# Performance work log

Measured on AMD Instinct MI355X. Metric: run time of the kernel, lower is better.

Reference implementation:

```python
import jax, jax.numpy as jnp
import numpy as np

HEADS = 8
DIM_HEAD = 64
LA = 0.33
LD = 0.33
LG = 0.33


def setup_inputs() -> dict:
    key = jax.random.key(0)
    ks = jax.random.split(key, 6)
    B, N, D = 4, 1024, 512
    inner = HEADS * DIM_HEAD
    x = jax.random.normal(ks[0], (B, N, D), jnp.float32)
    mask = jax.random.uniform(ks[1], (B, N)) < 0.9
    # sparse 0/1 molecular adjacency
    adjacency_mat = (jax.random.uniform(ks[2], (B, N, N)) < 0.05).astype(jnp.float32)
    # positive pairwise distances
    distance_mat = jax.random.uniform(ks[3], (B, N, N), jnp.float32) * 5.0
    W_qkv = jax.random.normal(ks[4], (D, inner * 3), jnp.float32) * 0.02
    W_out = jax.random.normal(ks[5], (inner, D), jnp.float32) * 0.02
    b_out = jnp.zeros((D,), jnp.float32)
    return {"x": x, "mask": mask, "adjacency_mat": adjacency_mat,
            "distance_mat": distance_mat, "W_qkv": W_qkv, "W_out": W_out, "b_out": b_out}


def reference(x, mask, adjacency_mat, distance_mat, W_qkv, W_out, b_out):
    B, N, _ = x.shape
    scale = DIM_HEAD ** -0.5
    # 'b n (h qkv d)' split: reshape to (B, N, H, 3, Dh) then move heads forward
    qkv = (x @ W_qkv).reshape(B, N, HEADS, 3, DIM_HEAD)
    q, k, v = (jnp.transpose(qkv[..., i, :], (0, 2, 1, 3)) for i in range(3))
    dots = jnp.einsum('bhid,bhjd->bhij', q, k) * scale  # [B,H,N,N]
    big = jnp.finfo(dots.dtype).max
    m2 = mask[:, None, :, None] & mask[:, None, None, :]  # [B,1,N,N]
    dots = jnp.where(m2, dots, -big)
    attn = jax.nn.softmax(dots, axis=-1) * LA
    # adjacency masked to 0; distance masked to +max so exp(-t) -> 0
    adj = jnp.where(m2, adjacency_mat[:, None], 0.0)
    dist = jnp.where(m2, distance_mat[:, None], big)
    attn = attn + LG * adj + LD * jnp.exp(-dist)
    out = jnp.einsum('bhij,bhjd->bhid', attn, v)
    out = jnp.transpose(out, (0, 2, 1, 3)).reshape(B, N, HEADS * DIM_HEAD)
    return out @ W_out + b_out
```

## Files before the change

### kernel.cpp

```cpp
#include <hip/hip_runtime.h>
#include <hip/hip_bf16.h>

typedef __attribute__((ext_vector_type(8))) __bf16 bf16x8;
typedef __attribute__((ext_vector_type(8))) unsigned short ushort8;
typedef __attribute__((ext_vector_type(4))) float f32x4;

#define DEVFN static __device__ __forceinline__

constexpr int B_ = 4, N_ = 1024, H_ = 8, DH_ = 64, INNER_ = 512, QC_ = 1536;
constexpr int JS_ = 2;
constexpr float LA_ = 0.33f, LD_ = 0.33f, LG_ = 0.33f;
constexpr float SCALE2_ = 0.125f * 1.44269504088896f;
constexpr long OCP_STRIDE_ = (long)4096 * 512;
constexpr long LP_STRIDE_  = (long)4 * 8 * 1024;

DEVFN unsigned short f2b(float f){
  unsigned int u = __builtin_bit_cast(unsigned int, f);
  u += 0x7FFFu + ((u >> 16) & 1u);
  return (unsigned short)(u >> 16);
}
DEVFN float b2f(unsigned short s){
  unsigned int u = ((unsigned int)s) << 16;
  return __builtin_bit_cast(float, u);
}
DEVFN float fexp2(float x){
  float r; asm("v_exp_f32 %0, %1" : "=v"(r) : "v"(x)); return r;
}
DEVFN unsigned int pack2(float lo, float hi){
  union { unsigned int u; __bf16 h[2]; } z;
  z.h[0] = (__bf16)lo; z.h[1] = (__bf16)hi;
  return z.u;
}

DEVFN f32x4 mfma16(bf16x8 a, bf16x8 b, f32x4 c){
  return __builtin_amdgcn_mfma_f32_16x16x32_bf16(a, b, c, 0, 0, 0);
}

DEVFN bf16x8 ldsb8(const unsigned short* p){ return *(const bf16x8*)p; }

DEVFN void gload16(const unsigned short* g, unsigned short* l){
  __builtin_amdgcn_global_load_lds(
      (const __attribute__((address_space(1))) unsigned int*)g,
      (__attribute__((address_space(3))) unsigned int*)l, 16, 0, 0);
}

DEVFN void lds_barrier(){
  __builtin_amdgcn_sched_barrier(0);
  asm volatile("s_waitcnt lgkmcnt(0)\n\ts_barrier" ::: "memory");
  __builtin_amdgcn_sched_barrier(0);
}


DEVFN int detect_enc_w0(const unsigned char* m8, const int* m32, const float* mf,
                        int t, int* fsh){
  if (t < 64){
    unsigned char a = m8[t];
    int bb = m32[t];
    float c = mf[t];
    unsigned long long bad0 = __ballot(a > 1);
    unsigned long long one0 = __ballot(a == 1);
    unsigned long long bad1 = __ballot(bb != 0 && bb != 1);
    unsigned long long one1 = __ballot(bb == 1);
    unsigned long long bad2 = __ballot(c != 0.0f && c != 1.0f);
    unsigned long long one2 = __ballot(c == 1.0f);
    if (t == 0){
      int f = 0;
      if (bad0 == 0ull && __popcll(one0) > 42) f = 0;
      else if (bad1 == 0ull && __popcll(one1) > 42) f = 1;
      else if (bad2 == 0ull && __popcll(one2) > 42) f = 2;
      *fsh = f;
    }
  }
  __syncthreads();
  return *fsh;
}

__global__ void prep_k(const unsigned char* __restrict__ m8, const int* __restrict__ m32,
                       const float* __restrict__ mf, unsigned char* __restrict__ mv,
                       const float* __restrict__ x, unsigned short* __restrict__ xb,
                       const float* __restrict__ Wq, unsigned short* __restrict__ WqT,
                       const float* __restrict__ Wo, unsigned short* __restrict__ WoT)
{
  const int bid = blockIdx.x, t = threadIdx.x;
  if (bid < 16){
    __shared__ int fsh;
    int f = detect_enc_w0(m8, m32, mf, t, &fsh);
    int i = bid * 256 + t;
    unsigned char v;
    if (f == 0) v = (m8[i] != 0);
    else if (f == 1) v = (m32[i] != 0);
    else v = (mf[i] != 0.0f);
    mv[i] = v;
  } else if (bid < 2064){
    int i = (bid - 16) * 256 + t;
    float4 v = ((const float4*)x)[i];
    ushort4 o = { f2b(v.x), f2b(v.y), f2b(v.z), f2b(v.w) };
    ((ushort4*)xb)[i] = o;
  } else {
    const float* W; unsigned short* Wt; int K, Nn, bx, by;
    if (bid < 2832){ W = Wq; Wt = WqT; K = 512; Nn = 1536; int r = bid - 2064; bx = r % 48; by = r / 48; }
    else           { W = Wo; Wt = WoT; K = 512; Nn = 512;  int r = bid - 2832; bx = r % 16; by = r / 16; }
    __shared__ float tt[32][33];
    int nb = bx * 32, kb = by * 32;
    int tx = t & 31, ty = t >> 5;
    #pragma unroll
    for (int i = 0; i < 32; i += 8)
      tt[ty + i][tx] = W[(long)(kb + ty + i) * Nn + nb + tx];
    __syncthreads();
    #pragma unroll
    for (int i = 0; i < 32; i += 8)
      Wt[(long)(nb + ty + i) * K + kb + tx] = f2b(tt[tx][ty + i]);
  }
}

template<int MODE, int BM, int BN>
__global__ __launch_bounds__(256)
void gemm_bt_k(const unsigned short* __restrict__ A, const unsigned short* __restrict__ Bt,
               const float* __restrict__ Cin, void* __restrict__ Cout,
               const unsigned short* __restrict__ Op, const float* __restrict__ Lp,
               unsigned short* __restrict__ VtOut,
               int M, int Nn, int K, long azs, long bzs)
{
  constexpr int BK = 64;
  constexpr int WM = BM / 2, WN = BN / 2, MR = WM / 16, NR = WN / 16;
  __shared__ __attribute__((aligned(16))) unsigned short As[2][BM * BK];
  __shared__ __attribute__((aligned(16))) unsigned short Bs[2][BN * BK];
  const int bm = blockIdx.x * BM, bn = blockIdx.y * BN, z = blockIdx.z;
  const unsigned short* Ap = A + (long)z * azs;
  const unsigned short* Bp = Bt + (long)z * bzs;
  const int tid = threadIdx.x, w = tid >> 6, lane = tid & 63;
  const int l15 = lane & 15, lg = lane >> 4;
  const int wr = w >> 1, wc = w & 1;
  const int srow = lane >> 3;
  const int sk0 = ((lane & 7) ^ srow) * 8;
  const int rk0 = (lg ^ (l15 & 7)) * 8;
  const int rk1 = ((lg + 4) ^ (l15 & 7)) * 8;

  f32x4 acc[MR][NR] = {};

  for (int kk = 0;;){
    if (kk == 0){
      #pragma unroll
      for (int i = 0; i < BM / 32; i++){
        int r0 = i * 32 + w * 8;
        gload16(Ap + (long)(bm + r0 + srow) * K + sk0, &As[0][r0 * BK]);
      }
      #pragma unroll
      for (int i = 0; i < BN / 32; i++){
        int r0 = i * 32 + w * 8;
        gload16(Bp + (long)(bn + r0 + srow) * K + sk0, &Bs[0][r0 * BK]);
      }
      __syncthreads();
    }
    int cur = (kk / BK) & 1;
    if (kk + BK < K){
      #pragma unroll
      for (int i = 0; i < BM / 32; i++){
        int r0 = i * 32 + w * 8;
        gload16(Ap + (long)(bm + r0 + srow) * K + (kk + BK) + sk0, &As[cur ^ 1][r0 * BK]);
      }
      #pragma unroll
      for (int i = 0; i < BN / 32; i++){
        int r0 = i * 32 + w * 8;
        gload16(Bp + (long)(bn + r0 + srow) * K + (kk + BK) + sk0, &Bs[cur ^ 1][r0 * BK]);
      }
    }
    bf16x8 af[MR][2], bf[NR][2];
    #pragma unroll
    for (int m = 0; m < MR; m++){
      const unsigned short* p = &As[cur][(wr * WM + m * 16 + l15) * BK];
      af[m][0] = ldsb8(p + rk0); af[m][1] = ldsb8(p + rk1);
    }
    #pragma unroll
    for (int n = 0; n < NR; n++){
      const unsigned short* p = &Bs[cur][(wc * WN + n * 16 + l15) * BK];
      bf[n][0] = ldsb8(p + rk0); bf[n][1] = ldsb8(p + rk1);
    }
    #pragma unroll
    for (int m = 0; m < MR; m++)
      #pragma unroll
      for (int n = 0; n < NR; n++){
        acc[m][n] = mfma16(af[m][0], bf[n][0], acc[m][n]);
        acc[m][n] = mfma16(af[m][1], bf[n][1], acc[m][n]);
      }
    kk += BK;
    if (kk >= K) break;
    __syncthreads();
  }

  #pragma unroll
  for (int m = 0; m < MR; m++)
    #pragma unroll
    for (int n = 0; n < NR; n++){
      int row0 = bm + wr * WM + m * 16 + lg * 4;
      int col = bn + wc * WN + n * 16 + l15;
      if (MODE == 0){
        ushort4 o;
        unsigned short* op = (unsigned short*)&o;
        #pragma unroll
        for (int r = 0; r < 4; r++){
          op[r] = f2b(acc[m][n][r]);
          ((unsigned short*)Cout)[(long)(row0 + r) * Nn + col] = op[r];
        }
        int hm = col % 192;
        if (hm >= 128){
          int bb = row0 >> 10, j0 = row0 & (N_ - 1);
          int hd = (col / 192) * 64 + (hm - 128);
          *(ushort4*)(VtOut + ((long)bb * INNER_ + hd) * N_ + j0) = o;
        }
      } else if (MODE == 1){
        #pragma unroll
        for (int r = 0; r < 4; r++){
          int row = row0 + r;
          float v = acc[m][n][r];
          long obase = ((long)z * N_ + row) * INNER_ + col;
          long lbase = ((long)z * H_ + (col >> 6)) * N_ + row;
          float o = 0.f, l = 0.f;
          #pragma unroll
          for (int js = 0; js < JS_; js++){
            o += b2f(Op[js * OCP_STRIDE_ + obase]);
            l += Lp[js * LP_STRIDE_ + lbase];
          }
          v += LA_ * o / l;
          ((unsigned short*)Cout)[((long)z * N_ + row) * Nn + col] = f2b(v);
        }
      } else {
        #pragma unroll
        for (int r = 0; r < 4; r++)
          ((float*)Cout)[(long)(row0 + r) * Nn + col] = acc[m][n][r] + Cin[col];
      }
    }
}

__global__ __launch_bounds__(256, 3)
void attn_madd_k(const unsigned short* __restrict__ QKV, const unsigned short* __restrict__ Vt,
                 const unsigned char* __restrict__ mv,
                 unsigned short* __restrict__ Ocp, float* __restrict__ Lp,
                 const unsigned char* __restrict__ m8, const int* __restrict__ m32,
                 const float* __restrict__ mf,
                 const float* __restrict__ adj, const float* __restrict__ dist,
                 unsigned short* __restrict__ Madd)
{
  __shared__ __attribute__((aligned(16))) unsigned short Ks[64][72];
  __shared__ __attribute__((aligned(16))) unsigned short Vs[64][72];
  __shared__ __attribute__((aligned(16))) unsigned short Ps[4][16][72];
  const int bid = blockIdx.x, tid = threadIdx.x;

  if (bid >= 512){
    int f = detect_enc_w0(m8, m32, mf, tid, (int*)&Ps[0][0][0]);
    long i = (long)(bid - 512) * 256 + tid;
    long e = i * 4;
    int b = (int)(e >> 20);
    int rem = (int)(e & (long)(N_ * N_ - 1));
    int row = rem >> 10, col0 = rem & (N_ - 1);
    float4 a = ((const float4*)adj)[i];
    float4 d = ((const float4*)dist)[i];
    bool mi, mc[4];
    if (f == 0){
      mi = m8[b * N_ + row] != 0;
      unsigned int pk = *(const unsigned int*)(m8 + b * N_ + col0);
      #pragma unroll
      for (int r = 0; r < 4; r++) mc[r] = ((pk >> (8 * r)) & 255u) != 0;
    } else if (f == 1){
      mi = m32[b * N_ + row] != 0;
      #pragma unroll
      for (int r = 0; r < 4; r++) mc[r] = m32[b * N_ + col0 + r] != 0;
    } else {
      mi = mf[b * N_ + row] != 0.0f;
      #pragma unroll
      for (int r = 0; r < 4; r++) mc[r] = mf[b * N_ + col0 + r] != 0.0f;
    }
    float va[4] = {a.x, a.y, a.z, a.w};
    float vd[4] = {d.x, d.y, d.z, d.w};
    ushort4 o;
    unsigned short* op = (unsigned short*)&o;
    #pragma unroll
    for (int r = 0; r < 4; r++){
      bool m2 = mi && mc[r];
      float v = m2 ? (LG_ * va[r] + LD_ * __expf(-vd[r])) : 0.0f;
      op[r] = f2b(v);
    }
    ((ushort4*)Madd)[i] = o;
    return;
  }

  const int qb = (bid & 7) * 128, h = (bid >> 3) & 7;
  const int zc = bid >> 6;
  const int b = zc & 3, js = zc >> 2;
  const int w = tid >> 6, lane = tid & 63;
  const int l15 = lane & 15, lg = lane >> 4;

  bf16x8 qf[2][2];
  bool rv[2];
  #pragma unroll
  for (int qg = 0; qg < 2; qg++){
    const long qr = (long)(b * N_ + qb + w * 32 + qg * 16 + l15) * QC_ + h * 192;
    qf[qg][0] = *(const bf16x8*)(QKV + qr + lg * 8);
    qf[qg][1] = *(const bf16x8*)(QKV + qr + 32 + lg * 8);
    rv[qg] = mv[b * N_ + qb + w * 32 + qg * 16 + l15] != 0;
  }

  float l_run[2] = {0.f, 0.f};
  f32x4 acc[2][4] = {};

  const unsigned short* Vbase = Vt + ((long)b * INNER_ + h * DH_) * N_;
  const unsigned short* Kbase = QKV + (long)b * N_ * QC_ + h * 192 + 64;
  const int kr0 = tid >> 3, kr1 = kr0 + 32;
  const int ko = (tid & 7) * 8;
  const int jb0 = js * (N_ / JS_);
  constexpr int NT = N_ / JS_ / 64;

  ushort8 kreg0, kreg1, vreg0, vreg1;
  {
    kreg0 = *(const ushort8*)(Kbase + (long)(jb0 + kr0) * QC_ + ko);
    kreg1 = *(const ushort8*)(Kbase + (long)(jb0 + kr1) * QC_ + ko);
    vreg0 = *(const ushort8*)(Vbase + (long)kr0 * N_ + jb0 + ko);
    vreg1 = *(const ushort8*)(Vbase + (long)kr1 * N_ + jb0 + ko);
  }

  for (int jt = 0; jt < NT; jt++){
    const int jbase = jb0 + jt * 64;
    lds_barrier();
    *(ushort8*)&Ks[kr0][ko] = kreg0;
    *(ushort8*)&Ks[kr1][ko] = kreg1;
    *(ushort8*)&Vs[kr0][ko] = vreg0;
    *(ushort8*)&Vs[kr1][ko] = vreg1;
    if (jt < NT - 1){
      const int jn = jbase + 64;
      kreg0 = *(const ushort8*)(Kbase + (long)(jn + kr0) * QC_ + ko);
      kreg1 = *(const ushort8*)(Kbase + (long)(jn + kr1) * QC_ + ko);
      vreg0 = *(const ushort8*)(Vbase + (long)kr0 * N_ + jn + ko);
      vreg1 = *(const ushort8*)(Vbase + (long)kr1 * N_ + jn + ko);
    }
    lds_barrier();

    bf16x8 kf[4][2];
    #pragma unroll
    for (int ct = 0; ct < 4; ct++){
      kf[ct][0] = ldsb8(&Ks[ct * 16 + l15][lg * 8]);
      kf[ct][1] = ldsb8(&Ks[ct * 16 + l15][32 + lg * 8]);
    }
    unsigned int cvm[4];
    #pragma unroll
    for (int ct = 0; ct < 4; ct++)
      cvm[ct] = *(const unsigned int*)(mv + b * N_ + jbase + ct * 16 + lg * 4);

    #pragma unroll
    for (int qg = 0; qg < 2; qg++){
      f32x4 s[4];
      __builtin_amdgcn_s_setprio(1);
      #pragma unroll
      for (int ct = 0; ct < 4; ct++){
        f32x4 zz = {};
        zz = mfma16(kf[ct][0], qf[qg][0], zz);
        zz = mfma16(kf[ct][1], qf[qg][1], zz);
        s[ct] = zz;
      }
      __builtin_amdgcn_s_setprio(0);

      float tsum = 0.f;
      unsigned int pw[4][2];
      #pragma unroll
      for (int ct = 0; ct < 4; ct++){
        float pv[4];
        #pragma unroll
        for (int r = 0; r < 4; r++){
          float xx = s[ct][r] * SCALE2_;
          bool ck = ((cvm[ct] >> (8 * r)) & 255u) != 0;
          float sv = ck ? xx : -3e38f;
          if (!rv[qg]) sv = 0.0f;
          float pp = fexp2(sv);
          tsum += pp;
          pv[r] = pp;
        }
        pw[ct][0] = pack2(pv[0], pv[1]);
        pw[ct][1] = pack2(pv[2], pv[3]);
      }
      tsum += __shfl_xor(tsum, 16);
      tsum += __shfl_xor(tsum, 32);
      l_run[qg] += tsum;

      asm volatile("s_waitcnt lgkmcnt(0)" ::: "memory");
      __builtin_amdgcn_sched_barrier(0);
      #pragma unroll
      for (int ct = 0; ct < 4; ct++)
        #pragma unroll
        for (int p2 = 0; p2 < 2; p2++){
          int klo = ct * 16 + lg * 4 + 2 * p2;
          *(unsigned int*)&Ps[w][l15][klo] = pw[ct][p2];
        }
      asm volatile("s_waitcnt lgkmcnt(0)" ::: "memory");
      __builtin_amdgcn_sched_barrier(0);

      bf16x8 pf0 = ldsb8(&Ps[w][l15][lg * 8]);
      bf16x8 pf1 = ldsb8(&Ps[w][l15][32 + lg * 8]);
      __builtin_amdgcn_s_setprio(1);
      #pragma unroll
      for (int ct = 0; ct < 4; ct++){
        bf16x8 v0 = ldsb8(&Vs[ct * 16 + l15][lg * 8]);
        bf16x8 v1 = ldsb8(&Vs[ct * 16 + l15][32 + lg * 8]);
        acc[qg][ct] = mfma16(pf0, v0, acc[qg][ct]);
        acc[qg][ct] = mfma16(pf1, v1, acc[qg][ct]);
      }
      __builtin_amdgcn_s_setprio(0);
    }
  }

  #pragma unroll
  for (int qg = 0; qg < 2; qg++){
    #pragma unroll
    for (int r = 0; r < 4; r++){
      long orow = (long)js * (OCP_STRIDE_ / INNER_) + b * N_ + qb + w * 32 + qg * 16 + lg * 4 + r;
      #pragma unroll
      for (int ct = 0; ct < 4; ct++)
        Ocp[orow * INNER_ + h * DH_ + ct * 16 + l15] = f2b(acc[qg][ct][r]);
    }
    if (lg == 0)
      Lp[(long)js * LP_STRIDE_ + ((long)b * H_ + h) * N_ + qb + w * 32 + qg * 16 + l15] = l_run[qg];
  }
}

extern "C" void kernel_launch(void* const* d_in, const int* in_sizes, int n_in,
                              void* d_out, int out_size, void* d_ws, size_t ws_size,
                              hipStream_t stream)
{
  const float* x    = (const float*)d_in[0];
  const void*  msk  = d_in[1];
  const float* adj  = (const float*)d_in[2];
  const float* dst  = (const float*)d_in[3];
  const float* wqkv = (const float*)d_in[4];
  const float* wout = (const float*)d_in[5];
  const float* bout = (const float*)d_in[6];
  float* out = (float*)d_out;

  char* p = (char*)d_ws;
  unsigned short* QKV  = (unsigned short*)p;  p += (long)4096 * 1536 * 2;
  unsigned short* Xb   = (unsigned short*)p;  p += (long)4096 * 512 * 2;
  unsigned short* WqT  = (unsigned short*)p;  p += (long)1536 * 512 * 2;
  unsigned short* WoT  = (unsigned short*)p;  p += (long)512 * 512 * 2;
  unsigned short* Vt   = (unsigned short*)p;  p += (long)4 * 512 * 1024 * 2;
  unsigned short* Madd = (unsigned short*)p;  p += (long)4 * 1024 * 1024 * 2;
  unsigned short* Ocp  = (unsigned short*)p;  p += (long)JS_ * OCP_STRIDE_ * 2;
  float*          Lp   = (float*)p;           p += (long)JS_ * LP_STRIDE_ * 4;
  unsigned short* OcB  = (unsigned short*)p;  p += (long)4096 * 512 * 2;
  unsigned char*  mv   = (unsigned char*)p;   p += 4096;

  prep_k<<<3088, 256, 0, stream>>>((const unsigned char*)msk, (const int*)msk,
                                   (const float*)msk, mv, x, Xb, wqkv, WqT, wout, WoT);
  gemm_bt_k<0, 128, 64><<<dim3(32, 24, 1), 256, 0, stream>>>(
      Xb, WqT, nullptr, QKV, nullptr, nullptr, Vt, 4096, 1536, 512, 0, 0);
  attn_madd_k<<<4608, 256, 0, stream>>>(QKV, Vt, mv, Ocp, Lp,
                                        (const unsigned char*)msk, (const int*)msk,
                                        (const float*)msk, adj, dst, Madd);
  gemm_bt_k<1, 64, 64><<<dim3(16, 8, 4), 256, 0, stream>>>(
      Madd, Vt, nullptr, OcB, Ocp, Lp, nullptr, 1024, 512, 1024,
      (long)1024 * 1024, (long)512 * 1024);
  gemm_bt_k<2, 64, 64><<<dim3(64, 8, 1), 256, 0, stream>>>(
      OcB, WoT, bout, out, nullptr, nullptr, nullptr, 4096, 512, 512, 0, 0);
}
```

Measured before the change: 70.57 us.

## Double-buffer K/V tiles via direct global-to-LDS loads with XOR swizzle

```diff
diff --git a/kernel.cpp b/kernel.cpp
--- a/kernel.cpp
+++ b/kernel.cpp
@@ -42,12 +42,6 @@
   __builtin_amdgcn_global_load_lds(
       (const __attribute__((address_space(1))) unsigned int*)g,
       (__attribute__((address_space(3))) unsigned int*)l, 16, 0, 0);
-}
-
-DEVFN void lds_barrier(){
-  __builtin_amdgcn_sched_barrier(0);
-  asm volatile("s_waitcnt lgkmcnt(0)\n\ts_barrier" ::: "memory");
-  __builtin_amdgcn_sched_barrier(0);
 }
 
 
@@ -241,8 +235,8 @@
                  const float* __restrict__ adj, const float* __restrict__ dist,
                  unsigned short* __restrict__ Madd)
 {
-  __shared__ __attribute__((aligned(16))) unsigned short Ks[64][72];
-  __shared__ __attribute__((aligned(16))) unsigned short Vs[64][72];
+  __shared__ __attribute__((aligned(16))) unsigned short Ks[2][64 * 64];
+  __shared__ __attribute__((aligned(16))) unsigned short Vs[2][64 * 64];
   __shared__ __attribute__((aligned(16))) unsigned short Ps[4][16][72];
   const int bid = blockIdx.x, tid = threadIdx.x;
 
@@ -305,40 +299,40 @@
 
   const unsigned short* Vbase = Vt + ((long)b * INNER_ + h * DH_) * N_;
   const unsigned short* Kbase = QKV + (long)b * N_ * QC_ + h * 192 + 64;
-  const int kr0 = tid >> 3, kr1 = kr0 + 32;
-  const int ko = (tid & 7) * 8;
   const int jb0 = js * (N_ / JS_);
   constexpr int NT = N_ / JS_ / 64;
 
-  ushort8 kreg0, kreg1, vreg0, vreg1;
-  {
-    kreg0 = *(const ushort8*)(Kbase + (long)(jb0 + kr0) * QC_ + ko);
-    kreg1 = *(const ushort8*)(Kbase + (long)(jb0 + kr1) * QC_ + ko);
-    vreg0 = *(const ushort8*)(Vbase + (long)kr0 * N_ + jb0 + ko);
-    vreg1 = *(const ushort8*)(Vbase + (long)kr1 * N_ + jb0 + ko);
-  }
+  const int srow = lane >> 3;
+  const int sk0 = ((lane & 7) ^ srow) * 8;
+  const int rk0 = (lg ^ (l15 & 7)) * 8;
+  const int rk1 = ((lg + 4) ^ (l15 & 7)) * 8;
+
+#define STAGE_TILE(JT, BUF)                                                   \
+  {                                                                           \
+    const int jb_ = jb0 + (JT) * 64;                                          \
+    _Pragma("unroll")                                                         \
+    for (int i = 0; i < 2; i++){                                              \
+      int r0 = i * 32 + w * 8;                                                \
+      gload16(Kbase + (long)(jb_ + r0 + srow) * QC_ + sk0, &Ks[BUF][r0 * 64]);\
+      gload16(Vbase + (long)(r0 + srow) * N_ + jb_ + sk0, &Vs[BUF][r0 * 64]); \
+    }                                                                         \
+  }
+
+  STAGE_TILE(0, 0)
+  __syncthreads();
 
   for (int jt = 0; jt < NT; jt++){
     const int jbase = jb0 + jt * 64;
-    lds_barrier();
-    *(ushort8*)&Ks[kr0][ko] = kreg0;
-    *(ushort8*)&Ks[kr1][ko] = kreg1;
-    *(ushort8*)&Vs[kr0][ko] = vreg0;
-    *(ushort8*)&Vs[kr1][ko] = vreg1;
-    if (jt < NT - 1){
-      const int jn = jbase + 64;
-      kreg0 = *(const ushort8*)(Kbase + (long)(jn + kr0) * QC_ + ko);
-      kreg1 = *(const ushort8*)(Kbase + (long)(jn + kr1) * QC_ + ko);
-      vreg0 = *(const ushort8*)(Vbase + (long)kr0 * N_ + jn + ko);
-      vreg1 = *(const ushort8*)(Vbase + (long)kr1 * N_ + jn + ko);
-    }
-    lds_barrier();
-
-    bf16x8 kf[4][2];
+    const int cur = jt & 1;
+    if (jt + 1 < NT) STAGE_TILE(jt + 1, cur ^ 1)
+
+    bf16x8 kf[4][2], vf[4][2];
     #pragma unroll
     for (int ct = 0; ct < 4; ct++){
-      kf[ct][0] = ldsb8(&Ks[ct * 16 + l15][lg * 8]);
-      kf[ct][1] = ldsb8(&Ks[ct * 16 + l15][32 + lg * 8]);
+      const unsigned short* pk = &Ks[cur][(ct * 16 + l15) * 64];
+      const unsigned short* pv = &Vs[cur][(ct * 16 + l15) * 64];
+      kf[ct][0] = ldsb8(pk + rk0); kf[ct][1] = ldsb8(pk + rk1);
+      vf[ct][0] = ldsb8(pv + rk0); vf[ct][1] = ldsb8(pv + rk1);
     }
     unsigned int cvm[4];
     #pragma unroll
@@ -397,14 +391,14 @@
       __builtin_amdgcn_s_setprio(1);
       #pragma unroll
       for (int ct = 0; ct < 4; ct++){
-        bf16x8 v0 = ldsb8(&Vs[ct * 16 + l15][lg * 8]);
-        bf16x8 v1 = ldsb8(&Vs[ct * 16 + l15][32 + lg * 8]);
-        acc[qg][ct] = mfma16(pf0, v0, acc[qg][ct]);
-        acc[qg][ct] = mfma16(pf1, v1, acc[qg][ct]);
+        acc[qg][ct] = mfma16(pf0, vf[ct][0], acc[qg][ct]);
+        acc[qg][ct] = mfma16(pf1, vf[ct][1], acc[qg][ct]);
       }
       __builtin_amdgcn_s_setprio(0);
     }
-  }
+    __syncthreads();
+  }
+#undef STAGE_TILE
 
   #pragma unroll
   for (int qg = 0; qg < 2; qg++){
```

Result: slower. 75.52 us (+7.0%).
